# Performance work log

Hardware: AMD Instinct MI355X
Metric: run time of the kernel (lower is better)

The kernel has to match this reference:

```python
import jax, jax.numpy as jnp
import numpy as np

MAX_ROUNDS = 6
MIN_ROUNDS = 2
WINDOW = 4
LAMBDA_P = 0.2
LN_EPS = 1e-5


def _mlp(x, W1, b1, W2, b2):
    # Linear -> exact GELU -> Linear (matches nn.Sequential(Linear, GELU, Linear))
    return jax.nn.gelu(x @ W1 + b1, approximate=False) @ W2 + b2


def _layernorm(x, g, b):
    m = x.mean(-1, keepdims=True)
    v = x.var(-1, keepdims=True)
    return (x - m) / jnp.sqrt(v + LN_EPS) * g + b


def setup_inputs() -> dict:
    key = jax.random.key(0)
    ks = jax.random.split(key, 13)
    B, N, D = 4, 2048, 512
    s = 0.02
    f32 = jnp.float32
    return {
        "summaries": jax.random.normal(ks[0], (B, N, D), f32),
        "msg_W1": jax.random.normal(ks[1], (2 * D, D), f32) * s,
        "msg_b1": jnp.zeros((D,), f32),
        "msg_W2": jax.random.normal(ks[2], (D, D), f32) * s,
        "msg_b2": jnp.zeros((D,), f32),
        "upd_W1": jax.random.normal(ks[3], (2 * D, D), f32) * s,
        "upd_b1": jnp.zeros((D,), f32),
        "upd_W2": jax.random.normal(ks[4], (D, D), f32) * s,
        "upd_b2": jnp.zeros((D,), f32),
        "halt_W": jax.random.normal(ks[5], (D, 1), f32) * s,
        "halt_b": jnp.zeros((1,), f32),
        "ln_g": jnp.ones((D,), f32),
        "ln_b": jnp.zeros((D,), f32),
    }


def reference(summaries, msg_W1, msg_b1, msg_W2, msg_b2,
              upd_W1, upd_b1, upd_W2, upd_b2,
              halt_W, halt_b, ln_g, ln_b):
    B, N, D = summaries.shape
    dt = summaries.dtype
    h = summaries
    remaining = jnp.ones((B, N, 1), dt)
    output = jnp.zeros_like(h)
    kl = jnp.zeros((), dt)
    done = jnp.asarray(False)  # emulates the early `break` under jit
    pos = jnp.arange(N)
    # number of valid causal neighbors of position i: min(i+1, window+1)
    counts = jnp.minimum(pos + 1, WINDOW + 1).astype(dt)[None, :, None]

    for step in range(MAX_ROUNDS):
        # windowed gather + message MLP, vectorized over the (W+1) offsets
        acc = jnp.zeros_like(h)
        for d in range(WINDOW + 1):
            nb = h if d == 0 else jnp.pad(h, ((0, 0), (d, 0), (0, 0)))[:, :N]
            m = _mlp(jnp.concatenate([h, nb], axis=-1), msg_W1, msg_b1, msg_W2, msg_b2)
            mask = (pos >= d).astype(dt)[None, :, None]
            acc = acc + m * mask
        msgs = acc / counts  # mean over valid neighbors, shape (B, N, D)

        new_h = h + _mlp(jnp.concatenate([h, msgs], axis=-1), upd_W1, upd_b1, upd_W2, upd_b2)
        h_next = _layernorm(new_h, ln_g, ln_b)

        if step < MIN_ROUNDS:
            halt = jnp.zeros((B, N, 1), dt)
        elif step == MAX_ROUNDS - 1:
            halt = jnp.ones((B, N, 1), dt)
        else:
            hp = jax.nn.sigmoid(h_next.mean(axis=1, keepdims=True) @ halt_W + halt_b)  # (B,1,1)
            halt = jnp.broadcast_to(hp, (B, N, 1))

        step_weight = remaining * halt
        out_next = output + step_weight * h_next
        rem_next = remaining * (1.0 - halt)

        p_geom = LAMBDA_P * (1.0 - LAMBDA_P) ** step
        # F.kl_div(log(q), log(p), log_target=True) = p * (log p - log q)
        kl_term = p_geom * (jnp.log(p_geom) - jnp.log(halt.mean() + 1e-8))

        active = jnp.logical_not(done)
        af = active.astype(dt)
        h = jnp.where(active, h_next, h)
        output = jnp.where(active, out_next, output)
        remaining = jnp.where(active, rem_next, remaining)
        kl = kl + af * kl_term.astype(dt)
        done = jnp.logical_or(done, remaining.max() < 0.01)

    return output, kl / MAX_ROUNDS
```

## Files before the change

kernel.cpp:

```cpp
#include <hip/hip_runtime.h>
#include <cmath>

#define DEV __device__ __forceinline__

typedef __bf16 bf16x8 __attribute__((ext_vector_type(8)));
typedef float f32x4v __attribute__((ext_vector_type(4)));
typedef unsigned short u16x8 __attribute__((ext_vector_type(8)));
typedef unsigned short u16x4 __attribute__((ext_vector_type(4)));

DEV float bf2f(unsigned short u){ return __uint_as_float(((unsigned)u)<<16); }
DEV unsigned short f2bf(float f){
  unsigned u = __float_as_uint(f);
  u = (u + 0x7fffu + ((u>>16)&1u)) >> 16;
  return (unsigned short)u;
}
DEV float geluf(float x){
  const float z = fabsf(x) * 0.70710678118654752f;
  const float t = __builtin_amdgcn_rcpf(1.0f + 0.3275911f*z);
  const float p = t*(0.254829592f + t*(-0.284496736f + t*(1.421413741f
                + t*(-1.453152027f + t*1.061405429f))));
  float er = 1.0f - p*__expf(-z*z);
  er = (x < 0.0f) ? -er : er;
  return 0.5f*x*(1.0f + er);
}

#define GLDS16(g,l) __builtin_amdgcn_global_load_lds(\
    (const __attribute__((address_space(1))) void*)(g), \
    (__attribute__((address_space(3))) void*)(l), 16, 0, 0)

#define NB    4
#define NSEQ  2048
#define DDIM  512
#define MROWS 8192

#define OFF_H     0u
#define OFF_HB    16777216u
#define OFF_UV    25165824u
#define OFF_GP    25165824u
#define OFF_R     33554432u
#define OFF_GSC   41943040u
#define OFF_WUV   50331648u
#define OFF_WP    51380224u
#define OFF_WR    52428800u
#define OFF_BUV   52953088u
#define OFF_BP    52957184u
#define OFF_BR    52959232u
#define OFF_DOT   52961280u
#define OFF_SCAL  52994048u
#define OFF_FLAGS 52994112u
#define OFF_A2    25165824u
#define OFF_B2    25690112u

__global__ __launch_bounds__(256) void k_prep_tr(
    const float* __restrict__ mW1, const float* __restrict__ uW2,
    const float* __restrict__ uW1,
    unsigned short* __restrict__ Wuv, unsigned short* __restrict__ Wr,
    unsigned short* __restrict__ Wp,  unsigned short* __restrict__ A2)
{
  __shared__ float t[64][65];
  const int tid = threadIdx.x, c = tid&63, r4 = tid>>6;
  const float* src; unsigned short* dst; int dld;
  switch (blockIdx.y){
    case 0: src = mW1;          dst = Wuv;          dld = 512;  break;
    case 1: src = mW1 + 262144; dst = Wuv + 262144; dld = 512;  break;
    case 2: src = uW2;          dst = Wr;           dld = 512;  break;
    case 3: src = uW1;          dst = Wp;           dld = 1024; break;
    default:src = uW1 + 262144; dst = A2;           dld = 512;  break;
  }
  const int k0 = (blockIdx.x>>3)<<6, n0 = (blockIdx.x&7)<<6;
  #pragma unroll
  for (int i=0;i<16;++i){ int r = i*4 + r4; t[r][c] = src[(size_t)(k0+r)*512 + n0 + c]; }
  __syncthreads();
  #pragma unroll
  for (int i=0;i<16;++i){ int r = i*4 + r4; dst[(size_t)(n0+r)*dld + k0 + c] = f2bf(t[c][r]); }
}

__global__ __launch_bounds__(256) void k_prep_small(
    const float* __restrict__ mW2, const float* __restrict__ mb1,
    const float* __restrict__ ub2,
    unsigned short* __restrict__ B2, float* __restrict__ biasUV,
    float* __restrict__ biasR)
{
  int idx = blockIdx.x*256 + threadIdx.x;
  if (idx < 262144)      B2[idx] = f2bf(mW2[idx]);
  else if (idx < 263168){ int j = idx-262144; biasUV[j] = (j<512)? mb1[j] : 0.f; }
  else if (idx < 263680){ int j = idx-263168; biasR[j] = ub2[j]; }
}

__global__ __launch_bounds__(256) void k_prep_biasP(
    const float* __restrict__ ub1, const float* __restrict__ mb2,
    const float* __restrict__ uW1, float* __restrict__ biasP)
{
  int n = blockIdx.x*256 + threadIdx.x;
  float s = ub1[n];
  for (int j=0;j<512;++j) s += mb2[j]*uW1[(512+j)*512+n];
  biasP[n] = s;
}

__global__ void k_init_state(float* scal, int* flags){
  int t = threadIdx.x;
  if (t<4) scal[t]=1.f;
  else if (t<9) scal[t]=0.f;
  if (t==9){ flags[0]=1; flags[1]=0; }
}

__global__ __launch_bounds__(256) void k_init_h(
    const float* __restrict__ S, float* __restrict__ H, u16x4* __restrict__ Hb)
{
  size_t idx = (size_t)blockIdx.x*256 + threadIdx.x;
  float4 v = ((const float4*)S)[idx];
  ((float4*)H)[idx] = v;
  u16x4 o; o[0]=f2bf(v.x); o[1]=f2bf(v.y); o[2]=f2bf(v.z); o[3]=f2bf(v.w);
  Hb[idx] = o;
}

template<int EPI>
__global__ __launch_bounds__(256) void k_gemm(
    const unsigned short* __restrict__ A0, const unsigned short* __restrict__ A1,
    const unsigned short* __restrict__ Bt, const float* __restrict__ bias,
    void* __restrict__ Cout, int ldc, int ldb, int nK, int ksplit, int gridN,
    const int* __restrict__ flags)
{
  if (flags[0]==0) return;
  __shared__ unsigned short sm[2][12288];
  const int tid = threadIdx.x;
  const int bid = blockIdx.x;
  const int nb  = (int)gridDim.x;
  const int ppx = (nb>>3)/gridN;
  int mp, np;
  if (ppx*gridN*8 == nb){ const int xcd = bid&7, ib = bid>>3; mp = xcd*ppx + ib/gridN; np = ib%gridN; }
  else                  { mp = bid/gridN; np = bid%gridN; }
  const int m0 = mp<<7, n0 = np<<6;
  const int sr = tid>>3;
  const int scA = (((tid&7) ^ (sr&7)) << 3);
  const int lane = tid&63, wv = tid>>6, wr = wv>>1, wc = wv&1;
  const int la = lane&15, lg = lane>>4;
  const int swzr = (la&7)<<3;
  f32x4v acc[4][2] = {};

  auto stage = [&](int ks, int bufi){
    const unsigned short* As = (ks<ksplit)? A0 : A1;
    const int kc = ((ks<ksplit)? ks : (ks-ksplit))<<6;
    unsigned short* s = sm[bufi];
    #pragma unroll
    for (int i=0;i<4;++i)
      GLDS16(As + (size_t)(m0 + i*32 + sr)*512 + kc + scA, s + i*2048 + tid*8);
    #pragma unroll
    for (int i=0;i<2;++i)
      GLDS16(Bt + (size_t)(n0 + i*32 + sr)*ldb + (ks<<6) + scA, s + 8192 + i*2048 + tid*8);
  };

  stage(0, 0);
  if (nK > 1) stage(1, 1);
  for (int ks=0; ks<nK; ++ks){
    const int cur = ks & 1;
    if (ks+1 < nK) asm volatile("s_waitcnt vmcnt(6)" ::: "memory");
    else           asm volatile("s_waitcnt vmcnt(0)" ::: "memory");
    __builtin_amdgcn_s_barrier();
    asm volatile("" ::: "memory");
    const unsigned short* s = sm[cur];
    #pragma unroll
    for (int kk=0;kk<2;++kk){
      bf16x8 af[4], bfr[2];
      #pragma unroll
      for (int mi=0;mi<4;++mi)
        af[mi] = *(const bf16x8*)(s + ((wr<<6) + (mi<<4) + la)*64 + (((kk<<5) + (lg<<3)) ^ swzr));
      #pragma unroll
      for (int ni=0;ni<2;++ni)
        bfr[ni] = *(const bf16x8*)(s + 8192 + ((wc<<5) + (ni<<4) + la)*64 + (((kk<<5) + (lg<<3)) ^ swzr));
      #pragma unroll
      for (int mi=0;mi<4;++mi)
        #pragma unroll
        for (int ni=0;ni<2;++ni)
          acc[mi][ni] = __builtin_amdgcn_mfma_f32_16x16x32_bf16(af[mi], bfr[ni], acc[mi][ni], 0, 0, 0);
    }
    asm volatile("" ::: "memory");
    __builtin_amdgcn_s_barrier();
    asm volatile("" ::: "memory");
    if (ks+2 < nK) stage(ks+2, cur);
  }

  const int r0 = m0 + (wr<<6) + (lg<<2);
  const int c0 = n0 + (wc<<5) + la;
  #pragma unroll
  for (int mi=0;mi<4;++mi){
    #pragma unroll
    for (int ni=0;ni<2;++ni){
      const int col = c0 + (ni<<4);
      const float bs = bias[col];
      #pragma unroll
      for (int r=0;r<4;++r){
        const int row = r0 + (mi<<4) + r;
        float v = acc[mi][ni][r] + bs;
        if constexpr (EPI==1) v = geluf(v);
        if constexpr (EPI==2) ((float*)Cout)[(size_t)row*ldc + col] = v;
        else ((unsigned short*)Cout)[(size_t)row*ldc + col] = f2bf(v);
      }
    }
  }
}

__global__ __launch_bounds__(256) void k_geluacc(
    const unsigned short* __restrict__ UV, unsigned short* __restrict__ G,
    const int* __restrict__ flags)
{
  if (flags[0]==0) return;
  int r = blockIdx.x*4 + (threadIdx.x>>6);
  int lane = threadIdx.x & 63;
  int c8 = lane*8;
  int i = r & (NSEQ-1);
  int nd = (i<4) ? i : 4;
  const u16x8 u = *(const u16x8*)(UV + (size_t)r*1024 + c8);
  float acc[8] = {0,0,0,0,0,0,0,0};
  for (int d=0; d<=nd; ++d){
    const u16x8 v = *(const u16x8*)(UV + (size_t)(r-d)*1024 + 512 + c8);
    #pragma unroll
    for (int j=0;j<8;++j) acc[j] += geluf(bf2f(u[j]) + bf2f(v[j]));
  }
  float inv = 1.0f/(float)(nd+1);
  u16x8 o;
  #pragma unroll
  for (int j=0;j<8;++j) o[j] = f2bf(acc[j]*inv);
  *(u16x8*)(G + (size_t)r*512 + c8) = o;
}

__global__ __launch_bounds__(256) void k_ln(
    const float* __restrict__ Rr, float* __restrict__ H, unsigned short* __restrict__ Hb,
    const float* __restrict__ gamma, const float* __restrict__ beta,
    const float* __restrict__ hW, float* __restrict__ DOT, float* __restrict__ OUT,
    const float* __restrict__ scal, const int* __restrict__ flags,
    int accmode, int dodot)
{
  const int lane = threadIdx.x & 63;
  const int row = (blockIdx.x<<2) + (threadIdx.x>>6);
  const int bidx = row >> 11;
  const size_t base = (size_t)row*512 + lane*8;
  float4 x0 = *(const float4*)(H+base);
  float4 x1 = *(const float4*)(H+base+4);

  if (accmode){
    const float w = scal[4+bidx];
    float4 o0, o1;
    if (accmode==1){
      o0 = make_float4(w*x0.x, w*x0.y, w*x0.z, w*x0.w);
      o1 = make_float4(w*x1.x, w*x1.y, w*x1.z, w*x1.w);
    } else {
      o0 = *(const float4*)(OUT+base);
      o1 = *(const float4*)(OUT+base+4);
      o0.x += w*x0.x; o0.y += w*x0.y; o0.z += w*x0.z; o0.w += w*x0.w;
      o1.x += w*x1.x; o1.y += w*x1.y; o1.z += w*x1.z; o1.w += w*x1.w;
    }
    *(float4*)(OUT+base)   = o0;
    *(float4*)(OUT+base+4) = o1;
  }
  if (flags[0]==0) return;

  float4 r0 = *(const float4*)(Rr+base);
  float4 r1 = *(const float4*)(Rr+base+4);
  x0.x+=r0.x; x0.y+=r0.y; x0.z+=r0.z; x0.w+=r0.w;
  x1.x+=r1.x; x1.y+=r1.y; x1.z+=r1.z; x1.w+=r1.w;
  float s = x0.x+x0.y+x0.z+x0.w + x1.x+x1.y+x1.z+x1.w;
  float q = x0.x*x0.x+x0.y*x0.y+x0.z*x0.z+x0.w*x0.w
          + x1.x*x1.x+x1.y*x1.y+x1.z*x1.z+x1.w*x1.w;
  #pragma unroll
  for (int off=1; off<64; off<<=1){ s += __shfl_xor(s, off); q += __shfl_xor(q, off); }
  const float mean = s*(1.f/512.f);
  const float var  = q*(1.f/512.f) - mean*mean;
  const float rstd = rsqrtf(var + 1e-5f);
  float4 g0 = *(const float4*)(gamma + lane*8);
  float4 g1 = *(const float4*)(gamma + lane*8 + 4);
  float4 b0 = *(const float4*)(beta  + lane*8);
  float4 b1 = *(const float4*)(beta  + lane*8 + 4);
  float y[8];
  y[0]=(x0.x-mean)*rstd*g0.x+b0.x; y[1]=(x0.y-mean)*rstd*g0.y+b0.y;
  y[2]=(x0.z-mean)*rstd*g0.z+b0.z; y[3]=(x0.w-mean)*rstd*g0.w+b0.w;
  y[4]=(x1.x-mean)*rstd*g1.x+b1.x; y[5]=(x1.y-mean)*rstd*g1.y+b1.y;
  y[6]=(x1.z-mean)*rstd*g1.z+b1.z; y[7]=(x1.w-mean)*rstd*g1.w+b1.w;
  *(float4*)(H+base)   = make_float4(y[0],y[1],y[2],y[3]);
  *(float4*)(H+base+4) = make_float4(y[4],y[5],y[6],y[7]);
  u16x8 hb;
  #pragma unroll
  for (int j=0;j<8;++j) hb[j] = f2bf(y[j]);
  *(u16x8*)(Hb+base) = hb;

  if (dodot){
    float4 w0 = *(const float4*)(hW + lane*8);
    float4 w1 = *(const float4*)(hW + lane*8 + 4);
    float d = y[0]*w0.x + y[1]*w0.y + y[2]*w0.z + y[3]*w0.w
            + y[4]*w1.x + y[5]*w1.y + y[6]*w1.z + y[7]*w1.w;
    #pragma unroll
    for (int off=1; off<64; off<<=1) d += __shfl_xor(d, off);
    if (lane==0) DOT[row] = d;
  }
}

__global__ void k_control(const float* __restrict__ DOT, const float* __restrict__ hb,
                          float* __restrict__ scal, int* __restrict__ flags,
                          int step, float p, float logp, float* __restrict__ klout)
{
  __shared__ float hp[4];
  const int t = threadIdx.x, lane = t&63, b = t>>6;
  if (step>=2 && step<5){
    float s = 0.f;
    for (int i=lane; i<NSEQ; i+=64) s += DOT[b*NSEQ + i];
    #pragma unroll
    for (int off=1; off<64; off<<=1) s += __shfl_xor(s, off);
    if (lane==0) hp[b] = s;
  } else if (lane==0) hp[b] = 0.f;
  __syncthreads();
  if (t==0){
    bool active = flags[0]!=0;
    float halt[NB];
    for (int i=0;i<NB;++i){
      if (step < 2) halt[i]=0.f;
      else if (step == 5) halt[i]=1.f;
      else { float z = hp[i]*(1.f/2048.f) + hb[0]; halt[i] = 1.f/(1.f+expf(-z)); }
    }
    float hm = 0.25f*(halt[0]+halt[1]+halt[2]+halt[3]);
    if (active) scal[8] += p*(logp - logf(hm + 1e-8f));
    float mx = 0.f;
    for (int i=0;i<NB;++i){
      float rb = scal[i];
      float w  = active ? rb*halt[i] : 0.f;
      scal[4+i] = w;
      if (active) rb *= (1.f - halt[i]);
      scal[i] = rb;
      mx = fmaxf(mx, rb);
    }
    if (mx < 0.01f) flags[1] = 1;
    flags[0] = flags[1] ? 0 : 1;
    if (step==5) *klout = scal[8]*(1.0f/6.0f);
  }
}

__global__ __launch_bounds__(256) void k_accum(
    const float* __restrict__ H, const float* __restrict__ scal, float* __restrict__ OUT)
{
  size_t idx = (size_t)blockIdx.x*256 + threadIdx.x;
  int b = (int)(idx >> 18);
  float w = scal[4+b];
  float4 h = ((const float4*)H)[idx];
  float4 o = ((float4*)OUT)[idx];
  ((float4*)OUT)[idx] = make_float4(o.x+w*h.x, o.y+w*h.y, o.z+w*h.z, o.w+w*h.w);
}

extern "C" void kernel_launch(void* const* d_in, const int* in_sizes, int n_in,
                              void* d_out, int out_size, void* d_ws, size_t ws_size,
                              hipStream_t stream)
{
  const float* S   = (const float*)d_in[0];
  const float* mW1 = (const float*)d_in[1];
  const float* mb1 = (const float*)d_in[2];
  const float* mW2 = (const float*)d_in[3];
  const float* mb2 = (const float*)d_in[4];
  const float* uW1 = (const float*)d_in[5];
  const float* ub1 = (const float*)d_in[6];
  const float* uW2 = (const float*)d_in[7];
  const float* ub2 = (const float*)d_in[8];
  const float* hW  = (const float*)d_in[9];
  const float* hb  = (const float*)d_in[10];
  const float* lng = (const float*)d_in[11];
  const float* lnb = (const float*)d_in[12];

  char* ws = (char*)d_ws;
  float*          H     = (float*)(ws + OFF_H);
  unsigned short* Hb    = (unsigned short*)(ws + OFF_HB);
  unsigned short* UV    = (unsigned short*)(ws + OFF_UV);
  unsigned short* GP    = (unsigned short*)(ws + OFF_GP);
  unsigned short* GSC   = (unsigned short*)(ws + OFF_GSC);
  float*          Rb    = (float*)(ws + OFF_R);
  unsigned short* Wuv   = (unsigned short*)(ws + OFF_WUV);
  unsigned short* Wp    = (unsigned short*)(ws + OFF_WP);
  unsigned short* Wr    = (unsigned short*)(ws + OFF_WR);
  unsigned short* A2    = (unsigned short*)(ws + OFF_A2);
  unsigned short* B2    = (unsigned short*)(ws + OFF_B2);
  float*          biasUV= (float*)(ws + OFF_BUV);
  float*          biasP = (float*)(ws + OFF_BP);
  float*          biasR = (float*)(ws + OFF_BR);
  float*          DOT   = (float*)(ws + OFF_DOT);
  float*          scal  = (float*)(ws + OFF_SCAL);
  int*            flags = (int*)(ws + OFF_FLAGS);
  float*          OUT   = (float*)d_out;
  float*          klout = OUT + (size_t)NB*NSEQ*DDIM;

  k_init_state<<<1, 256, 0, stream>>>(scal, flags);
  k_prep_tr   <<<dim3(64,5), 256, 0, stream>>>(mW1, uW2, uW1, Wuv, Wr, Wp, A2);
  k_prep_small<<<1032, 256, 0, stream>>>(mW2, mb1, ub2, B2, biasUV, biasR);
  k_prep_biasP<<<2,    256, 0, stream>>>(ub1, mb2, uW1, biasP);
  k_gemm<0><<<32, 256, 0, stream>>>(A2, A2, B2, biasUV+512, Wp+512, 1024, 512, 8, 8, 8, flags);
  k_init_h    <<<4096, 256, 0, stream>>>(S, H, (u16x4*)Hb);

  for (int s = 0; s < 6; ++s){
    k_gemm<0><<<1024, 256, 0, stream>>>(Hb, Hb, Wuv, biasUV, UV, 1024, 512, 8, 8, 16, flags);
    k_geluacc<<<2048, 256, 0, stream>>>(UV, GSC, flags);
    k_gemm<1><<<512, 256, 0, stream>>>(Hb, GSC, Wp, biasP, GP, 512, 1024, 16, 8, 8, flags);
    k_gemm<2><<<512, 256, 0, stream>>>(GP, GP, Wr, biasR, Rb, 512, 512, 8, 8, 8, flags);
    const int accmode = (s==3) ? 1 : (s>=4 ? 2 : 0);
    const int dodot   = (s>=2 && s<=4) ? 1 : 0;
    k_ln<<<2048, 256, 0, stream>>>(Rb, H, Hb, lng, lnb, hW, DOT, OUT, scal, flags, accmode, dodot);
    float p = 0.2f * (float)pow(0.8, (double)s);
    float lp = (float)log((double)p);
    k_control<<<1, 256, 0, stream>>>(DOT, hb, scal, flags, s, p, lp, klout);
  }
  k_accum<<<4096, 256, 0, stream>>>(H, scal, OUT);
}
```

Before: 553.9 us.

## Fuse halting control into LayerNorm via last-block counter and store residual as bf16

The per-step k_control launch is folded into k_ln: each block bumps a global atomic counter, and the last block to finish computes the halting probabilities, KL term and flags. The update-MLP output R is now written in bf16 instead of fp32, which halves that intermediate's write and read traffic. The prep kernels are merged into one launch to cut launch count. In exchange the residual add loses precision, and the kernel adds a threadfence and atomic per block.

```diff
diff --git a/kernel.cpp b/kernel.cpp
--- a/kernel.cpp
+++ b/kernel.cpp
@@ -48,6 +48,7 @@
 #define OFF_DOT   52961280u
 #define OFF_SCAL  52994048u
 #define OFF_FLAGS 52994112u
+#define OFF_CNT   52994176u
 #define OFF_A2    25165824u
 #define OFF_B2    25690112u
 
@@ -75,33 +76,32 @@
   for (int i=0;i<16;++i){ int r = i*4 + r4; dst[(size_t)(n0+r)*dld + k0 + c] = f2bf(t[c][r]); }
 }
 
-__global__ __launch_bounds__(256) void k_prep_small(
+__global__ __launch_bounds__(256) void k_prep_misc(
     const float* __restrict__ mW2, const float* __restrict__ mb1,
-    const float* __restrict__ ub2,
+    const float* __restrict__ ub2, const float* __restrict__ ub1,
+    const float* __restrict__ mb2, const float* __restrict__ uW1,
     unsigned short* __restrict__ B2, float* __restrict__ biasUV,
-    float* __restrict__ biasR)
-{
-  int idx = blockIdx.x*256 + threadIdx.x;
-  if (idx < 262144)      B2[idx] = f2bf(mW2[idx]);
-  else if (idx < 263168){ int j = idx-262144; biasUV[j] = (j<512)? mb1[j] : 0.f; }
-  else if (idx < 263680){ int j = idx-263168; biasR[j] = ub2[j]; }
-}
-
-__global__ __launch_bounds__(256) void k_prep_biasP(
-    const float* __restrict__ ub1, const float* __restrict__ mb2,
-    const float* __restrict__ uW1, float* __restrict__ biasP)
-{
-  int n = blockIdx.x*256 + threadIdx.x;
-  float s = ub1[n];
-  for (int j=0;j<512;++j) s += mb2[j]*uW1[(512+j)*512+n];
-  biasP[n] = s;
-}
-
-__global__ void k_init_state(float* scal, int* flags){
-  int t = threadIdx.x;
-  if (t<4) scal[t]=1.f;
-  else if (t<9) scal[t]=0.f;
-  if (t==9){ flags[0]=1; flags[1]=0; }
+    float* __restrict__ biasR, float* __restrict__ biasP,
+    float* __restrict__ scal, int* __restrict__ flags, unsigned* __restrict__ counter)
+{
+  const int bid = blockIdx.x, t = threadIdx.x;
+  if (bid < 1024){
+    int idx = bid*256 + t;
+    B2[idx] = f2bf(mW2[idx]);
+  } else if (bid == 1024){
+    for (int i=t;i<1024;i+=256) biasUV[i] = (i<512)? mb1[i] : 0.f;
+  } else if (bid == 1025){
+    for (int i=t;i<512;i+=256) biasR[i] = ub2[i];
+    if (t<4) scal[t]=1.f;
+    else if (t<9) scal[t]=0.f;
+    if (t==9){ flags[0]=1; flags[1]=0; }
+    if (t==10) *counter = 0u;
+  } else {
+    int n = (bid-1026)*256 + t;
+    float s = ub1[n];
+    for (int j=0;j<512;++j) s += mb2[j]*uW1[(512+j)*512+n];
+    biasP[n] = s;
+  }
 }
 
 __global__ __launch_bounds__(256) void k_init_h(
@@ -193,8 +193,7 @@
         const int row = r0 + (mi<<4) + r;
         float v = acc[mi][ni][r] + bs;
         if constexpr (EPI==1) v = geluf(v);
-        if constexpr (EPI==2) ((float*)Cout)[(size_t)row*ldc + col] = v;
-        else ((unsigned short*)Cout)[(size_t)row*ldc + col] = f2bf(v);
+        ((unsigned short*)Cout)[(size_t)row*ldc + col] = f2bf(v);
       }
     }
   }
@@ -225,16 +224,22 @@
 }
 
 __global__ __launch_bounds__(256) void k_ln(
-    const float* __restrict__ Rr, float* __restrict__ H, unsigned short* __restrict__ Hb,
+    const unsigned short* __restrict__ Rr, float* __restrict__ H, unsigned short* __restrict__ Hb,
     const float* __restrict__ gamma, const float* __restrict__ beta,
     const float* __restrict__ hW, float* __restrict__ DOT, float* __restrict__ OUT,
-    const float* __restrict__ scal, const int* __restrict__ flags,
-    int accmode, int dodot)
-{
-  const int lane = threadIdx.x & 63;
-  const int row = (blockIdx.x<<2) + (threadIdx.x>>6);
+    float* __restrict__ scal, int* __restrict__ flags, unsigned* __restrict__ counter,
+    const float* __restrict__ hb, float* __restrict__ klout,
+    int step, float p, float logp, int accmode, int dodot)
+{
+  __shared__ float hp[4];
+  __shared__ unsigned lastv;
+  const int tid = threadIdx.x;
+  const int lane = tid & 63;
+  const int row = (blockIdx.x<<2) + (tid>>6);
   const int bidx = row >> 11;
   const size_t base = (size_t)row*512 + lane*8;
+  const bool active = flags[0]!=0;
+
   float4 x0 = *(const float4*)(H+base);
   float4 x1 = *(const float4*)(H+base+4);
 
@@ -253,63 +258,65 @@
     *(float4*)(OUT+base)   = o0;
     *(float4*)(OUT+base+4) = o1;
   }
-  if (flags[0]==0) return;
-
-  float4 r0 = *(const float4*)(Rr+base);
-  float4 r1 = *(const float4*)(Rr+base+4);
-  x0.x+=r0.x; x0.y+=r0.y; x0.z+=r0.z; x0.w+=r0.w;
-  x1.x+=r1.x; x1.y+=r1.y; x1.z+=r1.z; x1.w+=r1.w;
-  float s = x0.x+x0.y+x0.z+x0.w + x1.x+x1.y+x1.z+x1.w;
-  float q = x0.x*x0.x+x0.y*x0.y+x0.z*x0.z+x0.w*x0.w
-          + x1.x*x1.x+x1.y*x1.y+x1.z*x1.z+x1.w*x1.w;
-  #pragma unroll
-  for (int off=1; off<64; off<<=1){ s += __shfl_xor(s, off); q += __shfl_xor(q, off); }
-  const float mean = s*(1.f/512.f);
-  const float var  = q*(1.f/512.f) - mean*mean;
-  const float rstd = rsqrtf(var + 1e-5f);
-  float4 g0 = *(const float4*)(gamma + lane*8);
-  float4 g1 = *(const float4*)(gamma + lane*8 + 4);
-  float4 b0 = *(const float4*)(beta  + lane*8);
-  float4 b1 = *(const float4*)(beta  + lane*8 + 4);
-  float y[8];
-  y[0]=(x0.x-mean)*rstd*g0.x+b0.x; y[1]=(x0.y-mean)*rstd*g0.y+b0.y;
-  y[2]=(x0.z-mean)*rstd*g0.z+b0.z; y[3]=(x0.w-mean)*rstd*g0.w+b0.w;
-  y[4]=(x1.x-mean)*rstd*g1.x+b1.x; y[5]=(x1.y-mean)*rstd*g1.y+b1.y;
-  y[6]=(x1.z-mean)*rstd*g1.z+b1.z; y[7]=(x1.w-mean)*rstd*g1.w+b1.w;
-  *(float4*)(H+base)   = make_float4(y[0],y[1],y[2],y[3]);
-  *(float4*)(H+base+4) = make_float4(y[4],y[5],y[6],y[7]);
-  u16x8 hb;
-  #pragma unroll
-  for (int j=0;j<8;++j) hb[j] = f2bf(y[j]);
-  *(u16x8*)(Hb+base) = hb;
-
-  if (dodot){
-    float4 w0 = *(const float4*)(hW + lane*8);
-    float4 w1 = *(const float4*)(hW + lane*8 + 4);
-    float d = y[0]*w0.x + y[1]*w0.y + y[2]*w0.z + y[3]*w0.w
-            + y[4]*w1.x + y[5]*w1.y + y[6]*w1.z + y[7]*w1.w;
-    #pragma unroll
-    for (int off=1; off<64; off<<=1) d += __shfl_xor(d, off);
-    if (lane==0) DOT[row] = d;
-  }
-}
-
-__global__ void k_control(const float* __restrict__ DOT, const float* __restrict__ hb,
-                          float* __restrict__ scal, int* __restrict__ flags,
-                          int step, float p, float logp, float* __restrict__ klout)
-{
-  __shared__ float hp[4];
-  const int t = threadIdx.x, lane = t&63, b = t>>6;
+
+  if (active){
+    const u16x8 rv = *(const u16x8*)(Rr+base);
+    x0.x+=bf2f(rv[0]); x0.y+=bf2f(rv[1]); x0.z+=bf2f(rv[2]); x0.w+=bf2f(rv[3]);
+    x1.x+=bf2f(rv[4]); x1.y+=bf2f(rv[5]); x1.z+=bf2f(rv[6]); x1.w+=bf2f(rv[7]);
+    float s = x0.x+x0.y+x0.z+x0.w + x1.x+x1.y+x1.z+x1.w;
+    float q = x0.x*x0.x+x0.y*x0.y+x0.z*x0.z+x0.w*x0.w
+            + x1.x*x1.x+x1.y*x1.y+x1.z*x1.z+x1.w*x1.w;
+    #pragma unroll
+    for (int off=1; off<64; off<<=1){ s += __shfl_xor(s, off); q += __shfl_xor(q, off); }
+    const float mean = s*(1.f/512.f);
+    const float var  = q*(1.f/512.f) - mean*mean;
+    const float rstd = rsqrtf(var + 1e-5f);
+    float4 g0 = *(const float4*)(gamma + lane*8);
+    float4 g1 = *(const float4*)(gamma + lane*8 + 4);
+    float4 b0 = *(const float4*)(beta  + lane*8);
+    float4 b1 = *(const float4*)(beta  + lane*8 + 4);
+    float y[8];
+    y[0]=(x0.x-mean)*rstd*g0.x+b0.x; y[1]=(x0.y-mean)*rstd*g0.y+b0.y;
+    y[2]=(x0.z-mean)*rstd*g0.z+b0.z; y[3]=(x0.w-mean)*rstd*g0.w+b0.w;
+    y[4]=(x1.x-mean)*rstd*g1.x+b1.x; y[5]=(x1.y-mean)*rstd*g1.y+b1.y;
+    y[6]=(x1.z-mean)*rstd*g1.z+b1.z; y[7]=(x1.w-mean)*rstd*g1.w+b1.w;
+    *(float4*)(H+base)   = make_float4(y[0],y[1],y[2],y[3]);
+    *(float4*)(H+base+4) = make_float4(y[4],y[5],y[6],y[7]);
+    u16x8 hbv;
+    #pragma unroll
+    for (int j=0;j<8;++j) hbv[j] = f2bf(y[j]);
+    *(u16x8*)(Hb+base) = hbv;
+
+    if (dodot){
+      float4 w0 = *(const float4*)(hW + lane*8);
+      float4 w1 = *(const float4*)(hW + lane*8 + 4);
+      float d = y[0]*w0.x + y[1]*w0.y + y[2]*w0.z + y[3]*w0.w
+              + y[4]*w1.x + y[5]*w1.y + y[6]*w1.z + y[7]*w1.w;
+      #pragma unroll
+      for (int off=1; off<64; off<<=1) d += __shfl_xor(d, off);
+      if (lane==0) DOT[row] = d;
+    }
+  }
+
+  __threadfence();
+  __syncthreads();
+  if (tid==0)
+    lastv = (atomicAdd(counter, 1u) == (unsigned)(gridDim.x-1)) ? 1u : 0u;
+  __syncthreads();
+  if (!lastv) return;
+
+  __threadfence();
+  if (tid==0) *counter = 0u;
+  const int b = tid>>6;
   if (step>=2 && step<5){
-    float s = 0.f;
-    for (int i=lane; i<NSEQ; i+=64) s += DOT[b*NSEQ + i];
-    #pragma unroll
-    for (int off=1; off<64; off<<=1) s += __shfl_xor(s, off);
-    if (lane==0) hp[b] = s;
+    float s2 = 0.f;
+    for (int i=lane; i<NSEQ; i+=64) s2 += DOT[(b<<11) + i];
+    #pragma unroll
+    for (int off=1; off<64; off<<=1) s2 += __shfl_xor(s2, off);
+    if (lane==0) hp[b] = s2;
   } else if (lane==0) hp[b] = 0.f;
   __syncthreads();
-  if (t==0){
-    bool active = flags[0]!=0;
+  if (tid==0){
     float halt[NB];
     for (int i=0;i<NB;++i){
       if (step < 2) halt[i]=0.f;
@@ -368,7 +375,7 @@
   unsigned short* UV    = (unsigned short*)(ws + OFF_UV);
   unsigned short* GP    = (unsigned short*)(ws + OFF_GP);
   unsigned short* GSC   = (unsigned short*)(ws + OFF_GSC);
-  float*          Rb    = (float*)(ws + OFF_R);
+  unsigned short* Rb16  = (unsigned short*)(ws + OFF_R);
   unsigned short* Wuv   = (unsigned short*)(ws + OFF_WUV);
   unsigned short* Wp    = (unsigned short*)(ws + OFF_WP);
   unsigned short* Wr    = (unsigned short*)(ws + OFF_WR);
@@ -380,27 +387,27 @@
   float*          DOT   = (float*)(ws + OFF_DOT);
   float*          scal  = (float*)(ws + OFF_SCAL);
   int*            flags = (int*)(ws + OFF_FLAGS);
+  unsigned*       cnt   = (unsigned*)(ws + OFF_CNT);
   float*          OUT   = (float*)d_out;
   float*          klout = OUT + (size_t)NB*NSEQ*DDIM;
 
-  k_init_state<<<1, 256, 0, stream>>>(scal, flags);
-  k_prep_tr   <<<dim3(64,5), 256, 0, stream>>>(mW1, uW2, uW1, Wuv, Wr, Wp, A2);
-  k_prep_small<<<1032, 256, 0, stream>>>(mW2, mb1, ub2, B2, biasUV, biasR);
-  k_prep_biasP<<<2,    256, 0, stream>>>(ub1, mb2, uW1, biasP);
+  k_prep_tr  <<<dim3(64,5), 256, 0, stream>>>(mW1, uW2, uW1, Wuv, Wr, Wp, A2);
+  k_prep_misc<<<1028, 256, 0, stream>>>(mW2, mb1, ub2, ub1, mb2, uW1,
+                                        B2, biasUV, biasR, biasP, scal, flags, cnt);
   k_gemm<0><<<32, 256, 0, stream>>>(A2, A2, B2, biasUV+512, Wp+512, 1024, 512, 8, 8, 8, flags);
-  k_init_h    <<<4096, 256, 0, stream>>>(S, H, (u16x4*)Hb);
+  k_init_h   <<<4096, 256, 0, stream>>>(S, H, (u16x4*)Hb);
 
   for (int s = 0; s < 6; ++s){
     k_gemm<0><<<1024, 256, 0, stream>>>(Hb, Hb, Wuv, biasUV, UV, 1024, 512, 8, 8, 16, flags);
     k_geluacc<<<2048, 256, 0, stream>>>(UV, GSC, flags);
     k_gemm<1><<<512, 256, 0, stream>>>(Hb, GSC, Wp, biasP, GP, 512, 1024, 16, 8, 8, flags);
-    k_gemm<2><<<512, 256, 0, stream>>>(GP, GP, Wr, biasR, Rb, 512, 512, 8, 8, 8, flags);
+    k_gemm<0><<<512, 256, 0, stream>>>(GP, GP, Wr, biasR, Rb16, 512, 512, 8, 8, 8, flags);
     const int accmode = (s==3) ? 1 : (s>=4 ? 2 : 0);
     const int dodot   = (s>=2 && s<=4) ? 1 : 0;
-    k_ln<<<2048, 256, 0, stream>>>(Rb, H, Hb, lng, lnb, hW, DOT, OUT, scal, flags, accmode, dodot);
-    float p = 0.2f * (float)pow(0.8, (double)s);
+    float p  = 0.2f * (float)pow(0.8, (double)s);
     float lp = (float)log((double)p);
-    k_control<<<1, 256, 0, stream>>>(DOT, hb, scal, flags, s, p, lp, klout);
+    k_ln<<<2048, 256, 0, stream>>>(Rb16, H, Hb, lng, lnb, hW, DOT, OUT,
+                                   scal, flags, cnt, hb, klout, s, p, lp, accmode, dodot);
   }
   k_accum<<<4096, 256, 0, stream>>>(H, scal, OUT);
 }
```

After: 1.945 ms. +251.2%, slower.
